# Performance work log

Hardware: AMD Instinct MI355X
Metric: run time of the kernel (lower is better)

## Reference

```python
import jax, jax.numpy as jnp
import numpy as np

B, L, M, H = 16, 1024, 1024, 128
NEG = -1e30


def setup_inputs() -> dict:
    key = jax.random.key(0)
    ks = jax.random.split(key, 8)
    return {
        "text": jax.random.normal(ks[0], (B, L, H), dtype=jnp.float32),
        "modality": jax.random.normal(ks[1], (B, M, H), dtype=jnp.float32),
        "text_mask": jax.random.randint(ks[2], (B, L), 0, 2, dtype=jnp.int32),
        "modality_mask": jax.random.randint(ks[3], (B, M), 0, 2, dtype=jnp.int32),
        # learned parameters (xavier-uniform style scale)
        "text_weight": jax.random.normal(ks[4], (H, 1), dtype=jnp.float32) * 0.1,
        "modality_weight": jax.random.normal(ks[5], (H, 1), dtype=jnp.float32) * 0.1,
        "text_modality_weight": jax.random.normal(ks[6], (1, 1, H), dtype=jnp.float32) * 0.1,
        "bias": jnp.zeros((1,), dtype=jnp.float32),
    }


def reference(text, modality, text_mask, modality_mask,
              text_weight, modality_weight, text_modality_weight, bias):
    # similarity matrix s: (B, L, M)   (eval mode: dropout is identity)
    s0 = jnp.matmul(text, text_weight)                      # (B, L, 1)
    s1 = jnp.swapaxes(jnp.matmul(modality, modality_weight), 1, 2)  # (B, 1, M)
    s2 = jnp.einsum('blh,bmh->blm', text * text_modality_weight, modality)
    s = s0 + s1 + s2 + bias                                 # (B, L, M)

    mmask = modality_mask[:, None, :].astype(jnp.float32)   # (B, 1, M)
    tmask = text_mask[:, :, None].astype(jnp.float32)       # (B, L, 1)
    p1 = jax.nn.softmax(mmask * s + (1.0 - mmask) * NEG, axis=2)  # text->modality
    p2 = jax.nn.softmax(tmask * s + (1.0 - tmask) * NEG, axis=1)  # modality->text

    a = jnp.matmul(p1, modality)                            # (B, L, H)
    b = jnp.matmul(jnp.matmul(p1, jnp.swapaxes(p2, 1, 2)), text)  # (B, L, H)
    return jnp.concatenate([text, a, text * a, text * b], axis=2)  # (B, L, 8H)
```

## Files before the change

### kernel.cpp

```cpp
#include <hip/hip_runtime.h>

#define B_ 16
#define L_ 1024
#define M_ 1024
#define H_ 128

typedef unsigned short u16;
typedef unsigned int u32;
typedef __bf16 bf16x8 __attribute__((ext_vector_type(8)));
typedef float f32x4 __attribute__((ext_vector_type(4)));

__device__ __forceinline__ u16 f2bf(float x){
  u32 u = __float_as_uint(x);
  u = (u + 0x7fffu + ((u >> 16) & 1u)) >> 16;
  return (u16)u;
}

__global__ __launch_bounds__(256) void zero_f32(float* __restrict__ p, int n)
{
  int i = blockIdx.x * 256 + threadIdx.x;
  if (i < n) p[i] = 0.f;
}

__global__ __launch_bounds__(256) void prep_rows(
    const float* __restrict__ src, const float* __restrict__ dotw,
    const float* __restrict__ mulw, u16* __restrict__ outbf,
    float* __restrict__ dotout, int nrows)
{
  int row = blockIdx.x * 4 + (threadIdx.x >> 6);
  int lane = threadIdx.x & 63;
  if (row >= nrows) return;
  const float* r = src + (size_t)row * H_;
  float2 x = *(const float2*)&r[lane * 2];
  float2 wv = *(const float2*)&dotw[lane * 2];
  float d = x.x * wv.x + x.y * wv.y;
  #pragma unroll
  for (int off = 32; off; off >>= 1) d += __shfl_xor(d, off);
  float2 mv = mulw ? *(const float2*)&mulw[lane * 2] : make_float2(1.f, 1.f);
  u32 packed = (u32)f2bf(x.x * mv.x) | ((u32)f2bf(x.y * mv.y) << 16);
  ((u32*)outbf)[(size_t)row * 64 + lane] = packed;
  if (lane == 0) dotout[row] = d;
}

__global__ __launch_bounds__(256) void transpose_bf(
    const float* __restrict__ srcA, const float* __restrict__ srcB,
    const int* __restrict__ maskA, const int* __restrict__ maskB,
    u16* __restrict__ dstA, u16* __restrict__ dstB)
{
  int b = blockIdx.z & 15, sel = blockIdx.z >> 4;
  const float* src = (sel ? srcB : srcA) + (size_t)b * L_ * H_;
  const int* msk = (sel ? maskB : maskA) + b * 1024;
  u16* dst = (sel ? dstB : dstA) + (size_t)b * H_ * L_;
  int r0 = blockIdx.x * 64, h0 = blockIdx.y * 64;
  __shared__ u16 tile[64][65];
  int t = threadIdx.x;
  int j = t & 63, i0 = t >> 6;
  #pragma unroll
  for (int p = 0; p < 16; p++) {
    int i = i0 + p * 4;
    tile[i][j] = msk[r0 + i] ? f2bf(src[(size_t)(r0 + i) * H_ + h0 + j]) : (u16)0;
  }
  __syncthreads();
  int ii = (t & 15) * 4, jj0 = t >> 4;
  #pragma unroll
  for (int q = 0; q < 4; q++) {
    int jj = jj0 + q * 16;
    u32 lo = (u32)tile[ii][jj] | ((u32)tile[ii + 1][jj] << 16);
    u32 hi = (u32)tile[ii + 2][jj] | ((u32)tile[ii + 3][jj] << 16);
    uint2 pk; pk.x = lo; pk.y = hi;
    *(uint2*)&dst[(size_t)(h0 + jj) * L_ + r0 + ii] = pk;
  }
}

__global__ __launch_bounds__(256) void gemm_exp(
    const u16* __restrict__ A, const u16* __restrict__ Bm,
    const float* __restrict__ t0, const float* __restrict__ s1m,
    const float* __restrict__ bias, const int* __restrict__ tmask,
    const int* __restrict__ mmask, float* __restrict__ rowsum,
    float* __restrict__ colsum, u16* __restrict__ ET)
{
  int b = blockIdx.z;
  int a0 = blockIdx.x * 64, b0 = blockIdx.y * 128;
  int tid = threadIdx.x, lane = tid & 63, wid = tid >> 6;
  int wr = wid >> 1, wc = wid & 1;
  int c = lane & 15, q = lane >> 4;
  __shared__ __align__(16) char smem[24576];
  const u16* Ab = A + (size_t)(b * L_ + a0) * H_;
  const u16* Bb = Bm + (size_t)(b * M_ + b0) * H_;
  f32x4 acc[2][4];
  #pragma unroll
  for (int i = 0; i < 2; i++)
    #pragma unroll
    for (int j = 0; j < 4; j++) acc[i][j] = (f32x4){0.f, 0.f, 0.f, 0.f};
  for (int kt = 0; kt < 2; kt++) {
    __syncthreads();
    #pragma unroll
    for (int i = 0; i < 2; i++) {
      int cc = tid + 256 * i;
      int row = cc >> 3, col8 = cc & 7;
      uint4 v = *(const uint4*)(Ab + (size_t)row * H_ + kt * 64 + col8 * 8);
      *(uint4*)(smem + row * 128 + ((col8 * 16) ^ ((row & 7) << 4))) = v;
    }
    #pragma unroll
    for (int i = 0; i < 4; i++) {
      int cc = tid + 256 * i;
      int row = cc >> 3, col8 = cc & 7;
      uint4 v = *(const uint4*)(Bb + (size_t)row * H_ + kt * 64 + col8 * 8);
      *(uint4*)(smem + 8192 + row * 128 + ((col8 * 16) ^ ((row & 7) << 4))) = v;
    }
    __syncthreads();
    #pragma unroll
    for (int kk = 0; kk < 2; kk++) {
      int kbyte = kk * 64 + (q << 4);
      bf16x8 af[2], bfr[4];
      #pragma unroll
      for (int i = 0; i < 2; i++) {
        int ra = wr * 32 + i * 16 + c;
        af[i] = *(const bf16x8*)(smem + ra * 128 + (kbyte ^ ((ra & 7) << 4)));
      }
      #pragma unroll
      for (int j = 0; j < 4; j++) {
        int rb = wc * 64 + j * 16 + c;
        bfr[j] = *(const bf16x8*)(smem + 8192 + rb * 128 + (kbyte ^ ((rb & 7) << 4)));
      }
      #pragma unroll
      for (int i = 0; i < 2; i++)
        #pragma unroll
        for (int j = 0; j < 4; j++)
          acc[i][j] = __builtin_amdgcn_mfma_f32_16x16x32_bf16(af[i], bfr[j], acc[i][j], 0, 0, 0);
    }
  }
  float biasv = bias[0];
  float t0v[2][4];
  int tmv[2][4];
  #pragma unroll
  for (int i = 0; i < 2; i++)
    #pragma unroll
    for (int r = 0; r < 4; r++) {
      int ar = a0 + wr * 32 + i * 16 + q * 4 + r;
      t0v[i][r] = t0[b * L_ + ar];
      tmv[i][r] = tmask[b * L_ + ar];
    }
  float s1v[4];
  int mmv[4];
  #pragma unroll
  for (int j = 0; j < 4; j++) {
    int gcol = b0 + wc * 64 + j * 16 + c;
    s1v[j] = s1m[b * M_ + gcol];
    mmv[j] = mmask[b * M_ + gcol];
  }
  float ev[2][4][4];
  #pragma unroll
  for (int i = 0; i < 2; i++)
    #pragma unroll
    for (int j = 0; j < 4; j++)
      #pragma unroll
      for (int r = 0; r < 4; r++)
        ev[i][j][r] = __expf(acc[i][j][r] + t0v[i][r] + s1v[j] + biasv);
  #pragma unroll
  for (int i = 0; i < 2; i++)
    #pragma unroll
    for (int r = 0; r < 4; r++) {
      float prs = 0.f;
      #pragma unroll
      for (int j = 0; j < 4; j++) prs += mmv[j] ? ev[i][j][r] : 0.f;
      #pragma unroll
      for (int off = 1; off < 16; off <<= 1) prs += __shfl_xor(prs, off);
      if (c == 0) {
        int ar = a0 + wr * 32 + i * 16 + q * 4 + r;
        atomicAdd(&rowsum[b * L_ + ar], prs);
      }
    }
  #pragma unroll
  for (int j = 0; j < 4; j++) {
    float pcs = 0.f;
    #pragma unroll
    for (int i = 0; i < 2; i++)
      #pragma unroll
      for (int r = 0; r < 4; r++) pcs += tmv[i][r] ? ev[i][j][r] : 0.f;
    pcs += __shfl_xor(pcs, 16);
    pcs += __shfl_xor(pcs, 32);
    if (q == 0) {
      int gcol = b0 + wc * 64 + j * 16 + c;
      atomicAdd(&colsum[b * M_ + gcol], pcs);
    }
  }
  __syncthreads();
  u16* et = (u16*)smem;
  #pragma unroll
  for (int i = 0; i < 2; i++)
    #pragma unroll
    for (int j = 0; j < 4; j++) {
      int gcolL = wc * 64 + j * 16 + c;
      int arL = wr * 32 + i * 16 + q * 4;
      u32 lo = (u32)f2bf(ev[i][j][0]) | ((u32)f2bf(ev[i][j][1]) << 16);
      u32 hi = (u32)f2bf(ev[i][j][2]) | ((u32)f2bf(ev[i][j][3]) << 16);
      uint2 pk; pk.x = lo; pk.y = hi;
      *(uint2*)&et[gcolL * 72 + arL] = pk;
    }
  __syncthreads();
  #pragma unroll
  for (int it = 0; it < 4; it++) {
    int mrow = (tid >> 3) + it * 32;
    int l8 = tid & 7;
    uint4 v = *(const uint4*)&et[mrow * 72 + l8 * 8];
    *(uint4*)&ET[((size_t)(b * M_ + b0 + mrow)) * L_ + a0 + l8 * 8] = v;
  }
}

__global__ __launch_bounds__(256) void gemm_ct(
    const u16* __restrict__ A, const u16* __restrict__ ET,
    const int* __restrict__ mmask, const float* __restrict__ colsum,
    u16* __restrict__ cT)
{
  int b = blockIdx.z;
  int a0 = blockIdx.x * 64, b0 = blockIdx.y * 128;
  int tid = threadIdx.x, lane = tid & 63, wid = tid >> 6;
  int wr = wid >> 1, wc = wid & 1;
  int c = lane & 15, q = lane >> 4;
  __shared__ __align__(16) char smem[24576];
  const u16* Ab = A + (size_t)(b * H_ + a0) * L_;
  const u16* Bb = ET + (size_t)(b * M_ + b0) * L_;
  f32x4 acc[2][4];
  #pragma unroll
  for (int i = 0; i < 2; i++)
    #pragma unroll
    for (int j = 0; j < 4; j++) acc[i][j] = (f32x4){0.f, 0.f, 0.f, 0.f};
  for (int kt = 0; kt < 16; kt++) {
    __syncthreads();
    #pragma unroll
    for (int i = 0; i < 2; i++) {
      int cc = tid + 256 * i;
      int row = cc >> 3, col8 = cc & 7;
      uint4 v = *(const uint4*)(Ab + (size_t)row * L_ + kt * 64 + col8 * 8);
      *(uint4*)(smem + row * 128 + ((col8 * 16) ^ ((row & 7) << 4))) = v;
    }
    #pragma unroll
    for (int i = 0; i < 4; i++) {
      int cc = tid + 256 * i;
      int row = cc >> 3, col8 = cc & 7;
      uint4 v = *(const uint4*)(Bb + (size_t)row * L_ + kt * 64 + col8 * 8);
      *(uint4*)(smem + 8192 + row * 128 + ((col8 * 16) ^ ((row & 7) << 4))) = v;
    }
    __syncthreads();
    #pragma unroll
    for (int kk = 0; kk < 2; kk++) {
      int kbyte = kk * 64 + (q << 4);
      bf16x8 af[2], bfr[4];
      #pragma unroll
      for (int i = 0; i < 2; i++) {
        int ra = wr * 32 + i * 16 + c;
        af[i] = *(const bf16x8*)(smem + ra * 128 + (kbyte ^ ((ra & 7) << 4)));
      }
      #pragma unroll
      for (int j = 0; j < 4; j++) {
        int rb = wc * 64 + j * 16 + c;
        bfr[j] = *(const bf16x8*)(smem + 8192 + rb * 128 + (kbyte ^ ((rb & 7) << 4)));
      }
      #pragma unroll
      for (int i = 0; i < 2; i++)
        #pragma unroll
        for (int j = 0; j < 4; j++)
          acc[i][j] = __builtin_amdgcn_mfma_f32_16x16x32_bf16(af[i], bfr[j], acc[i][j], 0, 0, 0);
    }
  }
  float invc[4];
  #pragma unroll
  for (int j = 0; j < 4; j++) {
    int gcol = b0 + wc * 64 + j * 16 + c;
    int mm = mmask[b * M_ + gcol];
    invc[j] = mm ? 1.0f / fmaxf(colsum[b * M_ + gcol], 1e-30f) : 0.f;
  }
  #pragma unroll
  for (int i = 0; i < 2; i++)
    #pragma unroll
    for (int j = 0; j < 4; j++) {
      int arow0 = a0 + wr * 32 + i * 16 + q * 4;
      int gcol = b0 + wc * 64 + j * 16 + c;
      #pragma unroll
      for (int r = 0; r < 4; r++)
        cT[((size_t)(b * H_ + arow0 + r)) * M_ + gcol] = f2bf(acc[i][j][r] * invc[j]);
    }
}

__global__ __launch_bounds__(256) void gemm_ab(
    const u16* __restrict__ ET, const u16* __restrict__ B1,
    const u16* __restrict__ B2, const float* __restrict__ rowsum,
    const float* __restrict__ text, float* __restrict__ out)
{
  int b = blockIdx.z;
  int a0 = blockIdx.x * 64;
  int tid = threadIdx.x, lane = tid & 63, wid = tid >> 6;
  int wr = wid >> 1, wc = wid & 1;
  int c = lane & 15, q = lane >> 4;
  __shared__ __align__(16) u16 At[64 * 76];
  __shared__ __align__(16) char Bs[2][16384];
  const u16* ETb = ET + (size_t)b * M_ * L_;
  const u16* B1b = B1 + (size_t)b * H_ * M_;
  const u16* B2b = B2 + (size_t)b * H_ * M_;
  f32x4 acc_a[2][4], acc_b[2][4];
  #pragma unroll
  for (int i = 0; i < 2; i++)
    #pragma unroll
    for (int j = 0; j < 4; j++) {
      acc_a[i][j] = (f32x4){0.f, 0.f, 0.f, 0.f};
      acc_b[i][j] = (f32x4){0.f, 0.f, 0.f, 0.f};
    }
  for (int kt = 0; kt < 16; kt++) {
    __syncthreads();
    #pragma unroll
    for (int it = 0; it < 2; it++) {
      int mloc = (tid >> 3) + it * 32;
      int l8 = tid & 7;
      uint4 v = *(const uint4*)&ETb[((size_t)(kt * 64 + mloc)) * L_ + a0 + l8 * 8];
      u16* rp = At + mloc * 76 + l8 * 8;
      uint2 p0; p0.x = v.x; p0.y = v.y;
      uint2 p1; p1.x = v.z; p1.y = v.w;
      *(uint2*)rp = p0;
      *(uint2*)(rp + 4) = p1;
    }
    #pragma unroll
    for (int i = 0; i < 4; i++) {
      int cc = tid + 256 * i;
      int row = cc >> 3, col8 = cc & 7;
      uint4 v1 = *(const uint4*)(B1b + (size_t)row * M_ + kt * 64 + col8 * 8);
      *(uint4*)(Bs[0] + row * 128 + ((col8 * 16) ^ ((row & 7) << 4))) = v1;
      uint4 v2 = *(const uint4*)(B2b + (size_t)row * M_ + kt * 64 + col8 * 8);
      *(uint4*)(Bs[1] + row * 128 + ((col8 * 16) ^ ((row & 7) << 4))) = v2;
    }
    __syncthreads();
    #pragma unroll
    for (int kk = 0; kk < 2; kk++) {
      int kbyte = kk * 64 + (q << 4);
      bf16x8 af[2], b1f[4], b2f[4];
      #pragma unroll
      for (int i = 0; i < 2; i++) {
        int lidx = wr * 32 + i * 16 + c;
        int mbase = kk * 32 + q * 8;
        union { unsigned short s[8]; bf16x8 v; } ua;
        #pragma unroll
        for (int e = 0; e < 8; e++) ua.s[e] = At[(mbase + e) * 76 + lidx];
        af[i] = ua.v;
      }
      #pragma unroll
      for (int j = 0; j < 4; j++) {
        int rb = wc * 64 + j * 16 + c;
        b1f[j] = *(const bf16x8*)(Bs[0] + rb * 128 + (kbyte ^ ((rb & 7) << 4)));
        b2f[j] = *(const bf16x8*)(Bs[1] + rb * 128 + (kbyte ^ ((rb & 7) << 4)));
      }
      #pragma unroll
      for (int i = 0; i < 2; i++)
        #pragma unroll
        for (int j = 0; j < 4; j++) {
          acc_a[i][j] = __builtin_amdgcn_mfma_f32_16x16x32_bf16(af[i], b1f[j], acc_a[i][j], 0, 0, 0);
          acc_b[i][j] = __builtin_amdgcn_mfma_f32_16x16x32_bf16(af[i], b2f[j], acc_b[i][j], 0, 0, 0);
        }
    }
  }
  float irs[2][4];
  #pragma unroll
  for (int i = 0; i < 2; i++)
    #pragma unroll
    for (int r = 0; r < 4; r++) {
      int ar = a0 + wr * 32 + i * 16 + q * 4 + r;
      irs[i][r] = 1.0f / fmaxf(rowsum[b * L_ + ar], 1e-30f);
    }
  #pragma unroll
  for (int i = 0; i < 2; i++)
    #pragma unroll
    for (int j = 0; j < 4; j++) {
      int gcol = wc * 64 + j * 16 + c;
      #pragma unroll
      for (int r = 0; r < 4; r++) {
        int ar = a0 + wr * 32 + i * 16 + q * 4 + r;
        float av = acc_a[i][j][r] * irs[i][r];
        float bv = acc_b[i][j][r] * irs[i][r];
        float tv = text[((size_t)(b * L_ + ar)) * H_ + gcol];
        size_t base = ((size_t)(b * L_ + ar)) * 512 + gcol;
        out[base] = tv;
        out[base + 128] = av;
        out[base + 256] = tv * av;
        out[base + 384] = tv * bv;
      }
    }
}

extern "C" void kernel_launch(void* const* d_in, const int* in_sizes, int n_in,
                              void* d_out, int out_size, void* d_ws, size_t ws_size,
                              hipStream_t stream) {
  const float* text = (const float*)d_in[0];
  const float* modality = (const float*)d_in[1];
  const int* text_mask = (const int*)d_in[2];
  const int* modality_mask = (const int*)d_in[3];
  const float* text_weight = (const float*)d_in[4];
  const float* modality_weight = (const float*)d_in[5];
  const float* tmw = (const float*)d_in[6];
  const float* bias = (const float*)d_in[7];
  float* out = (float*)d_out;
  (void)in_sizes; (void)n_in; (void)out_size; (void)ws_size;

  char* ws = (char*)d_ws;
  size_t off = 0;
  auto alloc = [&](size_t bytes) { void* p = ws + off; off += (bytes + 255) & ~(size_t)255; return p; };
  u16*   ET       = (u16*)  alloc((size_t)B_ * M_ * L_ * 2);
  u16*   textw_bf = (u16*)  alloc((size_t)B_ * L_ * H_ * 2);
  u16*   mod_bf   = (u16*)  alloc((size_t)B_ * M_ * H_ * 2);
  u16*   textT_bf = (u16*)  alloc((size_t)B_ * H_ * L_ * 2);
  u16*   mod_bfT  = (u16*)  alloc((size_t)B_ * H_ * M_ * 2);
  u16*   cT       = (u16*)  alloc((size_t)B_ * H_ * M_ * 2);
  float* t0       = (float*)alloc((size_t)B_ * L_ * 4);
  float* s1m      = (float*)alloc((size_t)B_ * M_ * 4);
  float* rowsum   = (float*)alloc((size_t)B_ * L_ * 4);
  float* colsum   = (float*)alloc((size_t)B_ * M_ * 4);

  zero_f32<<<128, 256, 0, stream>>>(rowsum, B_ * (L_ + M_));
  prep_rows<<<4096, 256, 0, stream>>>(text, text_weight, tmw, textw_bf, t0, B_ * L_);
  prep_rows<<<4096, 256, 0, stream>>>(modality, modality_weight, nullptr, mod_bf, s1m, B_ * M_);
  transpose_bf<<<dim3(16, 2, 32), 256, 0, stream>>>(text, modality, text_mask, modality_mask,
                                                    textT_bf, mod_bfT);
  gemm_exp<<<dim3(16, 8, 16), 256, 0, stream>>>(textw_bf, mod_bf, t0, s1m, bias,
      text_mask, modality_mask, rowsum, colsum, ET);
  gemm_ct<<<dim3(2, 8, 16), 256, 0, stream>>>(textT_bf, ET, modality_mask, colsum, cT);
  gemm_ab<<<dim3(16, 1, 16), 256, 0, stream>>>(ET, mod_bfT, cT, rowsum, text, out);
}
```

Measured before the change: 168.4 us.

## Split-K gemm_ct with atomics, widen GEMM blocks to 8 waves, remap grids

gemm_ct now splits its K dimension in two and accumulates fp32 partials with atomicAdd into a zeroed buffer. A separate norm_ct kernel then applies the column normalisation and the bf16 conversion. gemm_ct and gemm_ab move to 512-thread blocks, each wave taking a smaller 32-column tile, so there are more waves per tile. Block indices are linearised and swizzled so consecutive blocks spread across XCDs. The aim is more parallelism for the under-filled gemm_ct (256 blocks) and gemm_ab (256 blocks) launches. The cost is atomic traffic, an extra kernel, and a larger zero-fill.

```diff
diff --git a/kernel.cpp b/kernel.cpp
--- a/kernel.cpp
+++ b/kernel.cpp
@@ -16,10 +16,11 @@
   return (u16)u;
 }
 
-__global__ __launch_bounds__(256) void zero_f32(float* __restrict__ p, int n)
+__global__ __launch_bounds__(256) void zero_f32(float4* __restrict__ p, int n4)
 {
   int i = blockIdx.x * 256 + threadIdx.x;
-  if (i < n) p[i] = 0.f;
+  int stride = gridDim.x * 256;
+  for (; i < n4; i += stride) p[i] = make_float4(0.f, 0.f, 0.f, 0.f);
 }
 
 __global__ __launch_bounds__(256) void prep_rows(
@@ -79,8 +80,10 @@
     const int* __restrict__ mmask, float* __restrict__ rowsum,
     float* __restrict__ colsum, u16* __restrict__ ET)
 {
-  int b = blockIdx.z;
-  int a0 = blockIdx.x * 64, b0 = blockIdx.y * 128;
+  int f = blockIdx.x;
+  int orig = (f & 7) * 256 + (f >> 3);
+  int b = orig >> 7;
+  int a0 = (orig & 15) * 64, b0 = ((orig >> 4) & 7) * 128;
   int tid = threadIdx.x, lane = tid & 63, wid = tid >> 6;
   int wr = wid >> 1, wc = wid & 1;
   int c = lane & 15, q = lane >> 4;
@@ -208,36 +211,37 @@
   }
 }
 
-__global__ __launch_bounds__(256) void gemm_ct(
+__global__ __launch_bounds__(512) void gemm_ct(
     const u16* __restrict__ A, const u16* __restrict__ ET,
-    const int* __restrict__ mmask, const float* __restrict__ colsum,
-    u16* __restrict__ cT)
-{
-  int b = blockIdx.z;
-  int a0 = blockIdx.x * 64, b0 = blockIdx.y * 128;
+    float* __restrict__ c_f32)
+{
+  int f = blockIdx.x;
+  int orig = (f & 7) * 64 + (f >> 3);
+  int b = orig >> 5;
+  int x = orig & 3, y = (orig >> 2) & 7;
+  int ia = x & 1, ks = x >> 1;
+  int a0 = ia * 64, b0 = y * 128;
   int tid = threadIdx.x, lane = tid & 63, wid = tid >> 6;
-  int wr = wid >> 1, wc = wid & 1;
+  int wr = wid >> 2, wc = wid & 3;
   int c = lane & 15, q = lane >> 4;
   __shared__ __align__(16) char smem[24576];
   const u16* Ab = A + (size_t)(b * H_ + a0) * L_;
   const u16* Bb = ET + (size_t)(b * M_ + b0) * L_;
-  f32x4 acc[2][4];
-  #pragma unroll
-  for (int i = 0; i < 2; i++)
-    #pragma unroll
-    for (int j = 0; j < 4; j++) acc[i][j] = (f32x4){0.f, 0.f, 0.f, 0.f};
-  for (int kt = 0; kt < 16; kt++) {
-    __syncthreads();
-    #pragma unroll
-    for (int i = 0; i < 2; i++) {
-      int cc = tid + 256 * i;
-      int row = cc >> 3, col8 = cc & 7;
+  f32x4 acc[2][2];
+  #pragma unroll
+  for (int i = 0; i < 2; i++)
+    #pragma unroll
+    for (int j = 0; j < 2; j++) acc[i][j] = (f32x4){0.f, 0.f, 0.f, 0.f};
+  for (int kt = ks * 8; kt < ks * 8 + 8; kt++) {
+    __syncthreads();
+    {
+      int row = tid >> 3, col8 = tid & 7;
       uint4 v = *(const uint4*)(Ab + (size_t)row * L_ + kt * 64 + col8 * 8);
       *(uint4*)(smem + row * 128 + ((col8 * 16) ^ ((row & 7) << 4))) = v;
     }
     #pragma unroll
-    for (int i = 0; i < 4; i++) {
-      int cc = tid + 256 * i;
+    for (int i = 0; i < 2; i++) {
+      int cc = tid + 512 * i;
       int row = cc >> 3, col8 = cc & 7;
       uint4 v = *(const uint4*)(Bb + (size_t)row * L_ + kt * 64 + col8 * 8);
       *(uint4*)(smem + 8192 + row * 128 + ((col8 * 16) ^ ((row & 7) << 4))) = v;
@@ -246,72 +250,86 @@
     #pragma unroll
     for (int kk = 0; kk < 2; kk++) {
       int kbyte = kk * 64 + (q << 4);
-      bf16x8 af[2], bfr[4];
+      bf16x8 af[2], bfr[2];
       #pragma unroll
       for (int i = 0; i < 2; i++) {
         int ra = wr * 32 + i * 16 + c;
         af[i] = *(const bf16x8*)(smem + ra * 128 + (kbyte ^ ((ra & 7) << 4)));
       }
       #pragma unroll
-      for (int j = 0; j < 4; j++) {
-        int rb = wc * 64 + j * 16 + c;
+      for (int j = 0; j < 2; j++) {
+        int rb = wc * 32 + j * 16 + c;
         bfr[j] = *(const bf16x8*)(smem + 8192 + rb * 128 + (kbyte ^ ((rb & 7) << 4)));
       }
       #pragma unroll
       for (int i = 0; i < 2; i++)
         #pragma unroll
-        for (int j = 0; j < 4; j++)
+        for (int j = 0; j < 2; j++)
           acc[i][j] = __builtin_amdgcn_mfma_f32_16x16x32_bf16(af[i], bfr[j], acc[i][j], 0, 0, 0);
     }
   }
-  float invc[4];
-  #pragma unroll
-  for (int j = 0; j < 4; j++) {
-    int gcol = b0 + wc * 64 + j * 16 + c;
-    int mm = mmask[b * M_ + gcol];
-    invc[j] = mm ? 1.0f / fmaxf(colsum[b * M_ + gcol], 1e-30f) : 0.f;
-  }
-  #pragma unroll
-  for (int i = 0; i < 2; i++)
-    #pragma unroll
-    for (int j = 0; j < 4; j++) {
+  #pragma unroll
+  for (int i = 0; i < 2; i++)
+    #pragma unroll
+    for (int j = 0; j < 2; j++) {
       int arow0 = a0 + wr * 32 + i * 16 + q * 4;
-      int gcol = b0 + wc * 64 + j * 16 + c;
+      int gcol = b0 + wc * 32 + j * 16 + c;
       #pragma unroll
       for (int r = 0; r < 4; r++)
-        cT[((size_t)(b * H_ + arow0 + r)) * M_ + gcol] = f2bf(acc[i][j][r] * invc[j]);
-    }
-}
-
-__global__ __launch_bounds__(256) void gemm_ab(
+        atomicAdd(&c_f32[((size_t)(b * H_ + arow0 + r)) * M_ + gcol], acc[i][j][r]);
+    }
+}
+
+__global__ __launch_bounds__(256) void norm_ct(
+    const float* __restrict__ c_f32, const float* __restrict__ colsum,
+    const int* __restrict__ mmask, u16* __restrict__ cT)
+{
+  int g = blockIdx.x * 256 + threadIdx.x;
+  int base = g * 4;
+  int b = base >> 17;
+  int m = base & (M_ - 1);
+  float4 v = *(const float4*)&c_f32[base];
+  float4 cs = *(const float4*)&colsum[b * M_ + m];
+  int4 mm = *(const int4*)&mmask[b * M_ + m];
+  float o0 = mm.x ? v.x / fmaxf(cs.x, 1e-30f) : 0.f;
+  float o1 = mm.y ? v.y / fmaxf(cs.y, 1e-30f) : 0.f;
+  float o2 = mm.z ? v.z / fmaxf(cs.z, 1e-30f) : 0.f;
+  float o3 = mm.w ? v.w / fmaxf(cs.w, 1e-30f) : 0.f;
+  uint2 pk;
+  pk.x = (u32)f2bf(o0) | ((u32)f2bf(o1) << 16);
+  pk.y = (u32)f2bf(o2) | ((u32)f2bf(o3) << 16);
+  *(uint2*)&cT[base] = pk;
+}
+
+__global__ __launch_bounds__(512) void gemm_ab(
     const u16* __restrict__ ET, const u16* __restrict__ B1,
     const u16* __restrict__ B2, const float* __restrict__ rowsum,
     const float* __restrict__ text, float* __restrict__ out)
 {
-  int b = blockIdx.z;
-  int a0 = blockIdx.x * 64;
+  int f = blockIdx.x;
+  int orig = (f & 7) * 32 + (f >> 3);
+  int b = orig >> 4;
+  int a0 = (orig & 15) * 64;
   int tid = threadIdx.x, lane = tid & 63, wid = tid >> 6;
-  int wr = wid >> 1, wc = wid & 1;
+  int wr = wid >> 2, wc = wid & 3;
   int c = lane & 15, q = lane >> 4;
   __shared__ __align__(16) u16 At[64 * 76];
   __shared__ __align__(16) char Bs[2][16384];
   const u16* ETb = ET + (size_t)b * M_ * L_;
   const u16* B1b = B1 + (size_t)b * H_ * M_;
   const u16* B2b = B2 + (size_t)b * H_ * M_;
-  f32x4 acc_a[2][4], acc_b[2][4];
-  #pragma unroll
-  for (int i = 0; i < 2; i++)
-    #pragma unroll
-    for (int j = 0; j < 4; j++) {
+  f32x4 acc_a[2][2], acc_b[2][2];
+  #pragma unroll
+  for (int i = 0; i < 2; i++)
+    #pragma unroll
+    for (int j = 0; j < 2; j++) {
       acc_a[i][j] = (f32x4){0.f, 0.f, 0.f, 0.f};
       acc_b[i][j] = (f32x4){0.f, 0.f, 0.f, 0.f};
     }
   for (int kt = 0; kt < 16; kt++) {
     __syncthreads();
-    #pragma unroll
-    for (int it = 0; it < 2; it++) {
-      int mloc = (tid >> 3) + it * 32;
-      int l8 = tid & 7;
+    {
+      int mloc = tid >> 3, l8 = tid & 7;
       uint4 v = *(const uint4*)&ETb[((size_t)(kt * 64 + mloc)) * L_ + a0 + l8 * 8];
       u16* rp = At + mloc * 76 + l8 * 8;
       uint2 p0; p0.x = v.x; p0.y = v.y;
@@ -320,8 +338,8 @@
       *(uint2*)(rp + 4) = p1;
     }
     #pragma unroll
-    for (int i = 0; i < 4; i++) {
-      int cc = tid + 256 * i;
+    for (int i = 0; i < 2; i++) {
+      int cc = tid + 512 * i;
       int row = cc >> 3, col8 = cc & 7;
       uint4 v1 = *(const uint4*)(B1b + (size_t)row * M_ + kt * 64 + col8 * 8);
       *(uint4*)(Bs[0] + row * 128 + ((col8 * 16) ^ ((row & 7) << 4))) = v1;
@@ -332,7 +350,7 @@
     #pragma unroll
     for (int kk = 0; kk < 2; kk++) {
       int kbyte = kk * 64 + (q << 4);
-      bf16x8 af[2], b1f[4], b2f[4];
+      bf16x8 af[2], b1f[2], b2f[2];
       #pragma unroll
       for (int i = 0; i < 2; i++) {
         int lidx = wr * 32 + i * 16 + c;
@@ -343,15 +361,15 @@
         af[i] = ua.v;
       }
       #pragma unroll
-      for (int j = 0; j < 4; j++) {
-        int rb = wc * 64 + j * 16 + c;
+      for (int j = 0; j < 2; j++) {
+        int rb = wc * 32 + j * 16 + c;
         b1f[j] = *(const bf16x8*)(Bs[0] + rb * 128 + (kbyte ^ ((rb & 7) << 4)));
         b2f[j] = *(const bf16x8*)(Bs[1] + rb * 128 + (kbyte ^ ((rb & 7) << 4)));
       }
       #pragma unroll
       for (int i = 0; i < 2; i++)
         #pragma unroll
-        for (int j = 0; j < 4; j++) {
+        for (int j = 0; j < 2; j++) {
           acc_a[i][j] = __builtin_amdgcn_mfma_f32_16x16x32_bf16(af[i], b1f[j], acc_a[i][j], 0, 0, 0);
           acc_b[i][j] = __builtin_amdgcn_mfma_f32_16x16x32_bf16(af[i], b2f[j], acc_b[i][j], 0, 0, 0);
         }
@@ -368,8 +386,8 @@
   #pragma unroll
   for (int i = 0; i < 2; i++)
     #pragma unroll
-    for (int j = 0; j < 4; j++) {
-      int gcol = wc * 64 + j * 16 + c;
+    for (int j = 0; j < 2; j++) {
+      int gcol = wc * 32 + j * 16 + c;
       #pragma unroll
       for (int r = 0; r < 4; r++) {
         int ar = a0 + wr * 32 + i * 16 + q * 4 + r;
@@ -412,14 +430,17 @@
   float* s1m      = (float*)alloc((size_t)B_ * M_ * 4);
   float* rowsum   = (float*)alloc((size_t)B_ * L_ * 4);
   float* colsum   = (float*)alloc((size_t)B_ * M_ * 4);
-
-  zero_f32<<<128, 256, 0, stream>>>(rowsum, B_ * (L_ + M_));
+  float* c_f32    = (float*)alloc((size_t)B_ * H_ * M_ * 4);
+
+  int n4 = (B_ * (L_ + M_) + B_ * H_ * M_) / 4;
+  zero_f32<<<2048, 256, 0, stream>>>((float4*)rowsum, n4);
   prep_rows<<<4096, 256, 0, stream>>>(text, text_weight, tmw, textw_bf, t0, B_ * L_);
   prep_rows<<<4096, 256, 0, stream>>>(modality, modality_weight, nullptr, mod_bf, s1m, B_ * M_);
   transpose_bf<<<dim3(16, 2, 32), 256, 0, stream>>>(text, modality, text_mask, modality_mask,
                                                     textT_bf, mod_bfT);
-  gemm_exp<<<dim3(16, 8, 16), 256, 0, stream>>>(textw_bf, mod_bf, t0, s1m, bias,
+  gemm_exp<<<2048, 256, 0, stream>>>(textw_bf, mod_bf, t0, s1m, bias,
       text_mask, modality_mask, rowsum, colsum, ET);
-  gemm_ct<<<dim3(2, 8, 16), 256, 0, stream>>>(textT_bf, ET, modality_mask, colsum, cT);
-  gemm_ab<<<dim3(16, 1, 16), 256, 0, stream>>>(ET, mod_bfT, cT, rowsum, text, out);
-}
+  gemm_ct<<<512, 512, 0, stream>>>(textT_bf, ET, c_f32);
+  norm_ct<<<2048, 256, 0, stream>>>(c_f32, colsum, modality_mask, cT);
+  gemm_ab<<<256, 512, 0, stream>>>(ET, mod_bfT, cT, rowsum, text, out);
+}
```

Result: slower. 177.2 us (+5.3%).
